# Kernel tuning notes

Measured on AMD Instinct MI355X. Metric: run time of the kernel, lower is better.

Reference implementation:

```python
import jax, jax.numpy as jnp
import numpy as np

N = 100000   # nodes
E = 1600000  # edges
D_IN = 4
D_H = 128
EPS = 1e-5

def setup_inputs() -> dict:
    key = jax.random.key(0)
    ks = jax.random.split(key, 4)
    x = jax.random.normal(ks[0], (N, D_IN), dtype=jnp.float32)
    edge_index = jax.random.randint(ks[1], (2, E), 0, N, dtype=jnp.int32)
    W0 = jax.random.normal(ks[2], (D_IN, D_H), dtype=jnp.float32) * 0.5
    b0 = jnp.zeros((D_H,), jnp.float32)
    W12 = jax.random.normal(ks[3], (2, D_H, D_H), dtype=jnp.float32) * (1.0 / np.sqrt(D_H))
    b12 = jnp.zeros((2, D_H), jnp.float32)
    gamma = jnp.ones((3, D_H), jnp.float32)   # GraphNorm weight
    beta = jnp.zeros((3, D_H), jnp.float32)   # GraphNorm bias
    alpha = jnp.ones((3, D_H), jnp.float32)   # GraphNorm mean_scale
    return dict(x=x, edge_index=edge_index, W0=W0, b0=b0, W12=W12, b12=b12,
                gamma=gamma, beta=beta, alpha=alpha)

def gcn_conv(x, src, dst, dinv, W, b):
    # PyG GCNConv: linear first, then D^-1/2 (A+I) D^-1/2 aggregation, bias after.
    h = x @ W                                  # [N, d_out]
    coef = dinv[src] * dinv[dst]               # [E]
    msg = h[src] * coef[:, None]               # [E, d_out] gather
    agg = jax.ops.segment_sum(msg, dst, num_segments=N)  # scatter-add
    agg = agg + h * (dinv * dinv)[:, None]     # self-loop contribution
    return agg + b

def graph_norm(x, g, be, a):
    # single-graph GraphNorm: gamma*(x - alpha*mu)/sqrt(E[(x-alpha*mu)^2]+eps)+beta
    mu = x.mean(axis=0)
    xc = x - a * mu
    var = (xc * xc).mean(axis=0)
    return g * xc * jax.lax.rsqrt(var + EPS) + be

def reference(x, edge_index, W0, b0, W12, b12, gamma, beta, alpha):
    src, dst = edge_index[0], edge_index[1]
    # degree with self loops (edge weight 1)
    deg = jax.ops.segment_sum(jnp.ones((E,), x.dtype), dst, num_segments=N) + 1.0
    dinv = jax.lax.rsqrt(deg)
    h = jax.nn.relu(graph_norm(gcn_conv(x, src, dst, dinv, W0, b0),
                               gamma[0], beta[0], alpha[0]))
    for i in range(2):  # fixed small layer loop
        h = jax.nn.relu(graph_norm(gcn_conv(h, src, dst, dinv, W12[i], b12[i]),
                                   gamma[i + 1], beta[i + 1], alpha[i + 1]))
    return h
```

## Files before the change

### kernel.cpp

```cpp
#include <hip/hip_runtime.h>


#define EPS_GN 1e-5f

typedef __attribute__((ext_vector_type(8))) short bf16x8;
typedef __attribute__((ext_vector_type(4))) float f32x4;

__device__ __forceinline__ float blo(unsigned u) { return __uint_as_float(u << 16); }
__device__ __forceinline__ float bhi(unsigned u) { return __uint_as_float(u & 0xffff0000u); }
__device__ __forceinline__ unsigned bf16rne(float f) {
  unsigned u = __float_as_uint(f);
  u += 0x7fff + ((u >> 16) & 1);
  return u >> 16;
}
__device__ __forceinline__ unsigned packbf(float x, float y) {
  return bf16rne(x) | (bf16rne(y) << 16);
}


__global__ __launch_bounds__(256) void k_count_p(const int* __restrict__ dst,
                                                 int* __restrict__ cnt, int E, int N) {
  int p = blockIdx.x & 7;
  int lo = (int)((long long)N * p >> 3), hi = (int)((long long)N * (p + 1) >> 3);
  int stride = (gridDim.x >> 3) * 256;
  for (int e = (blockIdx.x >> 3) * 256 + threadIdx.x; e < E; e += stride) {
    int d = dst[e];
    if (d >= lo && d < hi) atomicAdd(&cnt[d], 1);
  }
}

__global__ __launch_bounds__(256) void k_scan1(const int* __restrict__ cnt,
                                               int* __restrict__ rs,
                                               int* __restrict__ bsum, int N) {
  __shared__ int s[256];
  int t = threadIdx.x;
  int base = blockIdx.x * 1024 + t * 4;
  int c0 = (base + 0 < N) ? cnt[base + 0] : 0;
  int c1 = (base + 1 < N) ? cnt[base + 1] : 0;
  int c2 = (base + 2 < N) ? cnt[base + 2] : 0;
  int c3 = (base + 3 < N) ? cnt[base + 3] : 0;
  int tsum = c0 + c1 + c2 + c3;
  s[t] = tsum;
  __syncthreads();
  for (int off = 1; off < 256; off <<= 1) {
    int v = (t >= off) ? s[t - off] : 0;
    __syncthreads();
    s[t] += v;
    __syncthreads();
  }
  int excl = s[t] - tsum;
  if (t == 255) bsum[blockIdx.x] = s[255];
  int e0 = excl, e1 = e0 + c0, e2 = e1 + c1, e3 = e2 + c2;
  if (base + 0 < N) rs[base + 0] = e0;
  if (base + 1 < N) rs[base + 1] = e1;
  if (base + 2 < N) rs[base + 2] = e2;
  if (base + 3 < N) rs[base + 3] = e3;
}

__global__ __launch_bounds__(256) void k_scan2(const int* __restrict__ bsum,
                                               int* __restrict__ boff, int nblk) {
  __shared__ int s[256];
  int t = threadIdx.x;
  int v0 = (t < nblk) ? bsum[t] : 0;
  s[t] = v0;
  __syncthreads();
  for (int off = 1; off < 256; off <<= 1) {
    int v = (t >= off) ? s[t - off] : 0;
    __syncthreads();
    s[t] += v;
    __syncthreads();
  }
  if (t < nblk) boff[t] = s[t] - v0;
}

__global__ __launch_bounds__(256) void k_finalize(const int* __restrict__ cnt,
                                                  const int* __restrict__ boff,
                                                  int* __restrict__ rs,
                                                  int* __restrict__ cursor,
                                                  float* __restrict__ dinv,
                                                  unsigned* __restrict__ Hcb, int N, int E,
                                                  int ROWS) {
  int i = blockIdx.x * 256 + threadIdx.x;
  if (i == 0) rs[N] = E;
  if (i < 64) Hcb[((size_t)(i >> 3) * ROWS + N) * 8 + (i & 7)] = 0u;
  if (i < N) {
    int v = rs[i] + boff[i >> 10];
    rs[i] = v;
    cursor[i] = v;
    dinv[i] = rsqrtf((float)cnt[i] + 1.0f);
  }
}

__global__ __launch_bounds__(256) void k_fill_p(const int* __restrict__ src,
                                                const int* __restrict__ dst,
                                                int* __restrict__ cursor,
                                                int* __restrict__ csr, int E, int N) {
  int p = blockIdx.x & 7;
  int lo = (int)((long long)N * p >> 3), hi = (int)((long long)N * (p + 1) >> 3);
  int stride = (gridDim.x >> 3) * 256;
  for (int e = (blockIdx.x >> 3) * 256 + threadIdx.x; e < E; e += stride) {
    int d = dst[e];
    if (d >= lo && d < hi) {
      int pos = atomicAdd(&cursor[d], 1);
      csr[pos] = src[e];
    }
  }
}


__global__ __launch_bounds__(256) void k_wt(const float* __restrict__ W12,
                                            unsigned short* __restrict__ WbT) {
  int o = blockIdx.x * 256 + threadIdx.x;
  int layer = o >> 14, r = o & 16383;
  int n = r >> 7, k = r & 127;
  WbT[o] = (unsigned short)bf16rne(W12[layer * 16384 + k * 128 + n]);
}


__global__ __launch_bounds__(256) void k_gemm0(const float* __restrict__ X,
                                               const float* __restrict__ W,
                                               const float* __restrict__ dinv,
                                               unsigned* __restrict__ Hcb, int N, int ROWS) {
  __shared__ float Ws[4 * 128];
  int t = threadIdx.x;
  if (t < 128) {
    Ws[t] = W[t];
    Ws[128 + t] = W[128 + t];
    Ws[256 + t] = W[256 + t];
    Ws[384 + t] = W[384 + t];
  }
  __syncthreads();
  int r = t >> 6, l = t & 63;
  int row = blockIdx.x * 4 + r;
  if (row >= N) return;
  float4 xv = ((const float4*)X)[row];
  float di = dinv[row];
  int c0 = 2 * l, c1 = 2 * l + 1;
  float v0 = xv.x * Ws[c0] + xv.y * Ws[128 + c0] + xv.z * Ws[256 + c0] + xv.w * Ws[384 + c0];
  float v1 = xv.x * Ws[c1] + xv.y * Ws[128 + c1] + xv.z * Ws[256 + c1] + xv.w * Ws[384 + c1];
  Hcb[((size_t)(l >> 3) * ROWS + row) * 8 + (l & 7)] = packbf(di * v0, di * v1);
}

__global__ __launch_bounds__(256, 4) void k_gemm_mfma(const unsigned* __restrict__ AGGcb,
                                                      const unsigned short* __restrict__ WbT,
                                                      const float* __restrict__ stats,
                                                      const float* __restrict__ bias,
                                                      const float* __restrict__ gamma,
                                                      const float* __restrict__ beta,
                                                      const float* __restrict__ alpha,
                                                      const float* __restrict__ dinv,
                                                      unsigned* __restrict__ Hcb, int N,
                                                      int ROWS, float invN) {
  __shared__ float As[128], Bs[128];
  int t = threadIdx.x;
  if (t < 128) {
    float s1 = stats[t] * invN, s2 = stats[128 + t] * invN;
    float b = bias[t], a = alpha[t], g = gamma[t], be = beta[t];
    float mu = s1 + b;
    float E2 = s2 + 2.f * b * s1 + b * b;
    float var = E2 - (2.f * a - a * a) * mu * mu;
    float A = g * rsqrtf(var + EPS_GN);
    As[t] = A;
    Bs[t] = be - A * a * mu + A * b;
  }
  __syncthreads();
  int wv = t >> 6, l = t & 63;
  int r0 = blockIdx.x * 64 + wv * 16;
  if (r0 >= N) return;
  int m = l & 15, kb = l >> 4;

  f32x4 acc[8];
#pragma unroll
  for (int nt = 0; nt < 8; ++nt) acc[nt] = (f32x4){0.f, 0.f, 0.f, 0.f};

#pragma unroll
  for (int ks = 0; ks < 4; ++ks) {
    int k0 = ks * 32 + kb * 8;
    const uint4* pa = (const uint4*)(AGGcb + ((size_t)(2 * ks + (kb >> 1)) * ROWS + r0 + m) * 8 +
                                     (kb & 1) * 4);
    uint4 a_raw = pa[0];
    float4 A0 = *reinterpret_cast<const float4*>(&As[k0]);
    float4 A1 = *reinterpret_cast<const float4*>(&As[k0 + 4]);
    float4 B0 = *reinterpret_cast<const float4*>(&Bs[k0]);
    float4 B1 = *reinterpret_cast<const float4*>(&Bs[k0 + 4]);
    bf16x8 bf[8];
#pragma unroll
    for (int nt = 0; nt < 8; ++nt)
      bf[nt] = *reinterpret_cast<const bf16x8*>(WbT + (size_t)(nt * 16 + m) * 128 + k0);
    float xr[8] = {blo(a_raw.x), bhi(a_raw.x), blo(a_raw.y), bhi(a_raw.y),
                   blo(a_raw.z), bhi(a_raw.z), blo(a_raw.w), bhi(a_raw.w)};
    float Aa[8] = {A0.x, A0.y, A0.z, A0.w, A1.x, A1.y, A1.z, A1.w};
    float Bb[8] = {B0.x, B0.y, B0.z, B0.w, B1.x, B1.y, B1.z, B1.w};
    bf16x8 af;
#pragma unroll
    for (int j = 0; j < 8; ++j) {
      float v = fmaf(Aa[j], xr[j], Bb[j]);
      v = v > 0.f ? v : 0.f;
      af[j] = (short)bf16rne(v);
    }
#pragma unroll
    for (int nt = 0; nt < 8; ++nt)
      acc[nt] = __builtin_amdgcn_mfma_f32_16x16x32_bf16(af, bf[nt], acc[nt], 0, 0, 0);
  }

  float dn[4];
#pragma unroll
  for (int r = 0; r < 4; ++r) dn[r] = dinv[r0 + kb * 4 + r];
  bool even = (l & 1) == 0;
#pragma unroll
  for (int nt = 0; nt < 8; ++nt) {
#pragma unroll
    for (int r = 0; r < 4; ++r) {
      float v = acc[nt][r] * dn[r];
      float pv = __shfl_xor(v, 1);
      if (even) {
        unsigned word = packbf(v, pv);
        Hcb[((size_t)nt * ROWS + r0 + kb * 4 + r) * 8 + (m >> 1)] = word;
      }
    }
  }
}

__global__ __launch_bounds__(256) void k_gather_cb(const unsigned* __restrict__ Hcb,
                                                   const int* __restrict__ rs,
                                                   const int* __restrict__ csr,
                                                   const float* __restrict__ dinv,
                                                   unsigned* __restrict__ AGGcb,
                                                   float* __restrict__ stats, int N, int ROWS) {
  int t = threadIdx.x;
  int wave = t >> 6, lane = t & 63;
  int g = lane >> 4, e = (lane >> 1) & 7, h = lane & 1;
  int p = blockIdx.x & 7;
  const uint4* Hp4 = (const uint4*)(Hcb + (size_t)p * ROWS * 8);
  uint4* Ap4 = (uint4*)(AGGcb + (size_t)p * ROWS * 8);
  int q = blockIdx.x >> 3;
  int nstride = (gridDim.x >> 3) * 16;
  float s1acc[8], s2acc[8];
#pragma unroll
  for (int i = 0; i < 8; ++i) s1acc[i] = s2acc[i] = 0.f;

  for (int n0 = (q * 4 + wave) * 4; n0 < N; n0 += nstride) {
    int n = n0 + g;
    int j0 = rs[n], j1 = rs[n + 1];
    int len = j1 - j0;
    int nb = (len + 8) >> 3;
    int ml = nb;
    ml = max(ml, __shfl_xor(ml, 16));
    ml = max(ml, __shfl_xor(ml, 32));
    float acc[8];
#pragma unroll
    for (int i = 0; i < 8; ++i) acc[i] = 0.f;

    auto ld = [&](int b) -> uint4 {
      int j = b * 8 + e - 1;
      int jj = j0 + j;
      jj = min(jj, j1 - 1);
      jj = max(jj, j0);
      int c = csr[jj];
      int r = (j < 0) ? n : ((j < len) ? c : N);
      return Hp4[(size_t)r * 2 + h];
    };

    uint4 rA = ld(0);
    uint4 rB, rC, rD, rE;
    if (ml > 1) rB = ld(1);
    if (ml > 2) rC = ld(2);
    if (ml > 3) rD = ld(3);
    for (int b = 0; b < ml; ++b) {
      if (b + 4 < ml) rE = ld(b + 4);
      unsigned uu[4] = {rA.x, rA.y, rA.z, rA.w};
#pragma unroll
      for (int i = 0; i < 4; ++i) {
        acc[2 * i] += blo(uu[i]);
        acc[2 * i + 1] += bhi(uu[i]);
      }
      rA = rB;
      rB = rC;
      rC = rD;
      rD = rE;
    }
#pragma unroll
    for (int i = 0; i < 8; ++i) {
      acc[i] += __shfl_xor(acc[i], 2);
      acc[i] += __shfl_xor(acc[i], 4);
      acc[i] += __shfl_xor(acc[i], 8);
    }
    if (e == 0) {
      float dn = dinv[n];
      float v[8];
      uint4 wv;
      unsigned* wp = (unsigned*)&wv;
#pragma unroll
      for (int i = 0; i < 8; ++i) v[i] = acc[i] * dn;
#pragma unroll
      for (int i = 0; i < 4; ++i) wp[i] = packbf(v[2 * i], v[2 * i + 1]);
      Ap4[(size_t)n * 2 + h] = wv;
#pragma unroll
      for (int i = 0; i < 8; ++i) {
        s1acc[i] += v[i];
        s2acc[i] = fmaf(v[i], v[i], s2acc[i]);
      }
    }
  }
#pragma unroll
  for (int i = 0; i < 8; ++i) {
    s1acc[i] += __shfl_xor(s1acc[i], 16);
    s1acc[i] += __shfl_xor(s1acc[i], 32);
    s2acc[i] += __shfl_xor(s2acc[i], 16);
    s2acc[i] += __shfl_xor(s2acc[i], 32);
  }
  __shared__ float sh[4][32];
  if (lane < 2) {
#pragma unroll
    for (int i = 0; i < 8; ++i) {
      sh[wave][h * 8 + i] = s1acc[i];
      sh[wave][16 + h * 8 + i] = s2acc[i];
    }
  }
  __syncthreads();
  if (t < 32) {
    float v = sh[0][t] + sh[1][t] + sh[2][t] + sh[3][t];
    if (t < 16)
      atomicAdd(&stats[p * 16 + t], v);
    else
      atomicAdd(&stats[128 + p * 16 + (t - 16)], v);
  }
}

__global__ __launch_bounds__(256) void k_norm(const unsigned* __restrict__ AGGcb,
                                              const float* __restrict__ stats,
                                              const float* __restrict__ bias,
                                              const float* __restrict__ gamma,
                                              const float* __restrict__ beta,
                                              const float* __restrict__ alpha,
                                              float* __restrict__ OUT, int N, int ROWS,
                                              float invN) {
  int i = blockIdx.x * 256 + threadIdx.x;
  if (i >= N * 32) return;
  int row = i >> 5, c4 = i & 31;
  int blk = c4 >> 2, off = (2 * c4) & 7;
  uint2 u = *(const uint2*)(AGGcb + ((size_t)blk * ROWS + row) * 8 + off);
  float vv[4] = {blo(u.x), bhi(u.x), blo(u.y), bhi(u.y)};
  float ov[4];
#pragma unroll
  for (int j = 0; j < 4; ++j) {
    int c = c4 * 4 + j;
    float s1 = stats[c] * invN, s2 = stats[128 + c] * invN;
    float b = bias[c], a = alpha[c], g = gamma[c], be = beta[c];
    float mu = s1 + b;
    float E2 = s2 + 2.f * b * s1 + b * b;
    float var = E2 - (2.f * a - a * a) * mu * mu;
    float A = g * rsqrtf(var + EPS_GN);
    float B = be - A * a * mu + A * b;
    float o = fmaf(A, vv[j], B);
    ov[j] = o > 0.f ? o : 0.f;
  }
  ((float4*)OUT)[i] = make_float4(ov[0], ov[1], ov[2], ov[3]);
}


extern "C" void kernel_launch(void* const* d_in, const int* in_sizes, int n_in,
                              void* d_out, int out_size, void* d_ws, size_t ws_size,
                              hipStream_t stream) {
  const float* x = (const float*)d_in[0];
  const int* ei = (const int*)d_in[1];
  const float* W0 = (const float*)d_in[2];
  const float* b0 = (const float*)d_in[3];
  const float* W12 = (const float*)d_in[4];
  const float* b12 = (const float*)d_in[5];
  const float* gamma = (const float*)d_in[6];
  const float* beta = (const float*)d_in[7];
  const float* alpha = (const float*)d_in[8];
  float* out = (float*)d_out;

  int N = in_sizes[0] / 4;
  int E = in_sizes[1] / 2;
  int ROWS = N + 1;
  const int* srcArr = ei;
  const int* dstArr = ei + E;

  char* w = (char*)d_ws;
  auto alloc = [&](size_t bytes) {
    char* p = w;
    w += (bytes + 255) & ~(size_t)255;
    return p;
  };
  int* cnt = (int*)alloc((size_t)N * 4);
  float* stats = (float*)alloc(3 * 256 * 4);
  int* rs = (int*)alloc(((size_t)N + 1) * 4);
  int* cursor = (int*)alloc((size_t)N * 4);
  int* bsum = (int*)alloc(512);
  int* boff = (int*)alloc(512);
  unsigned short* WbT = (unsigned short*)alloc(2 * 16384 * 2);
  int* csr = (int*)alloc(((size_t)E + 8) * 4);
  float* dinv = (float*)alloc((size_t)N * 4);
  unsigned* Hcb = (unsigned*)alloc((size_t)ROWS * 64 * 4);
  unsigned* AGGcb = (unsigned*)alloc((size_t)ROWS * 64 * 4);

  size_t zlen = (size_t)((char*)stats - (char*)cnt) + 3 * 256 * 4;
  hipMemsetAsync(cnt, 0, zlen, stream);

  int nblk = (N + 1023) / 1024;
  k_wt<<<128, 256, 0, stream>>>(W12, WbT);
  k_count_p<<<2048, 256, 0, stream>>>(dstArr, cnt, E, N);
  k_scan1<<<nblk, 256, 0, stream>>>(cnt, rs, bsum, N);
  k_scan2<<<1, 256, 0, stream>>>(bsum, boff, nblk);
  k_finalize<<<(N + 255) / 256, 256, 0, stream>>>(cnt, boff, rs, cursor, dinv, Hcb, N, E, ROWS);
  k_fill_p<<<2048, 256, 0, stream>>>(srcArr, dstArr, cursor, csr, E, N);

  float invN = 1.0f / (float)N;
  int gGemm = (N + 63) / 64;

  k_gemm0<<<(N + 3) / 4, 256, 0, stream>>>(x, W0, dinv, Hcb, N, ROWS);
  k_gather_cb<<<2048, 256, 0, stream>>>(Hcb, rs, csr, dinv, AGGcb, stats, N, ROWS);
  k_gemm_mfma<<<gGemm, 256, 0, stream>>>(AGGcb, WbT, stats, b0, gamma, beta, alpha, dinv, Hcb, N,
                                         ROWS, invN);
  k_gather_cb<<<2048, 256, 0, stream>>>(Hcb, rs, csr, dinv, AGGcb, stats + 256, N, ROWS);
  k_gemm_mfma<<<gGemm, 256, 0, stream>>>(AGGcb, WbT + 16384, stats + 256, b12, gamma + 128,
                                         beta + 128, alpha + 128, dinv, Hcb, N, ROWS, invN);
  k_gather_cb<<<2048, 256, 0, stream>>>(Hcb, rs, csr, dinv, AGGcb, stats + 512, N, ROWS);
  k_norm<<<(N * 32 + 255) / 256, 256, 0, stream>>>(AGGcb, stats + 512, b12 + 128, gamma + 256,
                                                   beta + 256, alpha + 256, out, N, ROWS, invN);
}
```

Before: 720.1 us.

## Pad CSR rows to multiples of eight with self-loop and sentinel entries

```diff
diff --git a/kernel.cpp b/kernel.cpp
--- a/kernel.cpp
+++ b/kernel.cpp
@@ -35,10 +35,10 @@
   __shared__ int s[256];
   int t = threadIdx.x;
   int base = blockIdx.x * 1024 + t * 4;
-  int c0 = (base + 0 < N) ? cnt[base + 0] : 0;
-  int c1 = (base + 1 < N) ? cnt[base + 1] : 0;
-  int c2 = (base + 2 < N) ? cnt[base + 2] : 0;
-  int c3 = (base + 3 < N) ? cnt[base + 3] : 0;
+  int c0 = (base + 0 < N) ? ((cnt[base + 0] + 8) & ~7) : 0;
+  int c1 = (base + 1 < N) ? ((cnt[base + 1] + 8) & ~7) : 0;
+  int c2 = (base + 2 < N) ? ((cnt[base + 2] + 8) & ~7) : 0;
+  int c3 = (base + 3 < N) ? ((cnt[base + 3] + 8) & ~7) : 0;
   int tsum = c0 + c1 + c2 + c3;
   s[t] = tsum;
   __syncthreads();
@@ -78,23 +78,37 @@
                                                   int* __restrict__ rs,
                                                   int* __restrict__ cursor,
                                                   float* __restrict__ dinv,
-                                                  unsigned* __restrict__ Hcb, int N, int E,
+                                                  unsigned* __restrict__ Hcb,
+                                                  int* __restrict__ csrp, int N, int E,
                                                   int ROWS) {
+  __shared__ int sTail;
   int i = blockIdx.x * 256 + threadIdx.x;
-  if (i == 0) rs[N] = E;
   if (i < 64) Hcb[((size_t)(i >> 3) * ROWS + N) * 8 + (i & 7)] = 0u;
   if (i < N) {
     int v = rs[i] + boff[i >> 10];
+    int c = cnt[i];
+    int pc = (c + 8) & ~7;
     rs[i] = v;
-    cursor[i] = v;
-    dinv[i] = rsqrtf((float)cnt[i] + 1.0f);
+    cursor[i] = v + 1;
+    dinv[i] = rsqrtf((float)c + 1.0f);
+    csrp[v] = i;
+    for (int k = v + 1 + c; k < v + pc; ++k) csrp[k] = N;
+    if (i == N - 1) {
+      rs[N] = v + pc;
+      sTail = v + pc;
+    }
+  }
+  __syncthreads();
+  if (blockIdx.x == gridDim.x - 1) {
+    int base = sTail;
+    for (int k = threadIdx.x; k < 1024; k += 256) csrp[base + k] = N;
   }
 }
 
 __global__ __launch_bounds__(256) void k_fill_p(const int* __restrict__ src,
                                                 const int* __restrict__ dst,
                                                 int* __restrict__ cursor,
-                                                int* __restrict__ csr, int E, int N) {
+                                                int* __restrict__ csrp, int E, int N) {
   int p = blockIdx.x & 7;
   int lo = (int)((long long)N * p >> 3), hi = (int)((long long)N * (p + 1) >> 3);
   int stride = (gridDim.x >> 3) * 256;
@@ -102,7 +116,7 @@
     int d = dst[e];
     if (d >= lo && d < hi) {
       int pos = atomicAdd(&cursor[d], 1);
-      csr[pos] = src[e];
+      csrp[pos] = src[e];
     }
   }
 }
@@ -222,8 +236,8 @@
 }
 
 __global__ __launch_bounds__(256) void k_gather_cb(const unsigned* __restrict__ Hcb,
-                                                   const int* __restrict__ rs,
-                                                   const int* __restrict__ csr,
+                                                   const int* __restrict__ rsp,
+                                                   const int* __restrict__ csrp,
                                                    const float* __restrict__ dinv,
                                                    unsigned* __restrict__ AGGcb,
                                                    float* __restrict__ stats, int N, int ROWS) {
@@ -241,9 +255,8 @@
 
   for (int n0 = (q * 4 + wave) * 4; n0 < N; n0 += nstride) {
     int n = n0 + g;
-    int j0 = rs[n], j1 = rs[n + 1];
-    int len = j1 - j0;
-    int nb = (len + 8) >> 3;
+    int j0 = rsp[n], j1 = rsp[n + 1];
+    int nb = (j1 - j0) >> 3;
     int ml = nb;
     ml = max(ml, __shfl_xor(ml, 16));
     ml = max(ml, __shfl_xor(ml, 32));
@@ -251,33 +264,39 @@
 #pragma unroll
     for (int i = 0; i < 8; ++i) acc[i] = 0.f;
 
-    auto ld = [&](int b) -> uint4 {
-      int j = b * 8 + e - 1;
-      int jj = j0 + j;
-      jj = min(jj, j1 - 1);
-      jj = max(jj, j0);
-      int c = csr[jj];
-      int r = (j < 0) ? n : ((j < len) ? c : N);
-      return Hp4[(size_t)r * 2 + h];
+    const int* cp = csrp + j0 + e;
+    auto hload = [&](int c, int b) -> uint4 {
+      int ce = (b < nb) ? c : N;
+      return Hp4[(size_t)ce * 2 + h];
     };
-
-    uint4 rA = ld(0);
-    uint4 rB, rC, rD, rE;
-    if (ml > 1) rB = ld(1);
-    if (ml > 2) rC = ld(2);
-    if (ml > 3) rD = ld(3);
-    for (int b = 0; b < ml; ++b) {
-      if (b + 4 < ml) rE = ld(b + 4);
-      unsigned uu[4] = {rA.x, rA.y, rA.z, rA.w};
-#pragma unroll
-      for (int i = 0; i < 4; ++i) {
-        acc[2 * i] += blo(uu[i]);
-        acc[2 * i + 1] += bhi(uu[i]);
+    int c0 = cp[0], c1 = cp[8];
+    uint4 hA = hload(c0, 0);
+    uint4 hB = hload(c1, 1);
+    int c2 = cp[16], c3 = cp[24];
+    const int* cpp = cp + 32;
+
+    for (int b = 0; b < ml; b += 2) {
+      {
+        unsigned uu[4] = {hA.x, hA.y, hA.z, hA.w};
+#pragma unroll
+        for (int i = 0; i < 4; ++i) {
+          acc[2 * i] += blo(uu[i]);
+          acc[2 * i + 1] += bhi(uu[i]);
+        }
       }
-      rA = rB;
-      rB = rC;
-      rC = rD;
-      rD = rE;
+      hA = hload(c2, b + 2);
+      c2 = cpp[0];
+      if (b + 1 < ml) {
+        unsigned uu[4] = {hB.x, hB.y, hB.z, hB.w};
+#pragma unroll
+        for (int i = 0; i < 4; ++i) {
+          acc[2 * i] += blo(uu[i]);
+          acc[2 * i + 1] += bhi(uu[i]);
+        }
+        hB = hload(c3, b + 3);
+        c3 = cpp[8];
+      }
+      cpp += 16;
     }
 #pragma unroll
     for (int i = 0; i < 8; ++i) {
@@ -392,7 +411,7 @@
   int* bsum = (int*)alloc(512);
   int* boff = (int*)alloc(512);
   unsigned short* WbT = (unsigned short*)alloc(2 * 16384 * 2);
-  int* csr = (int*)alloc(((size_t)E + 8) * 4);
+  int* csrp = (int*)alloc(((size_t)E + 8 * (size_t)N + 2048) * 4);
   float* dinv = (float*)alloc((size_t)N * 4);
   unsigned* Hcb = (unsigned*)alloc((size_t)ROWS * 64 * 4);
   unsigned* AGGcb = (unsigned*)alloc((size_t)ROWS * 64 * 4);
@@ -405,20 +424,21 @@
   k_count_p<<<2048, 256, 0, stream>>>(dstArr, cnt, E, N);
   k_scan1<<<nblk, 256, 0, stream>>>(cnt, rs, bsum, N);
   k_scan2<<<1, 256, 0, stream>>>(bsum, boff, nblk);
-  k_finalize<<<(N + 255) / 256, 256, 0, stream>>>(cnt, boff, rs, cursor, dinv, Hcb, N, E, ROWS);
-  k_fill_p<<<2048, 256, 0, stream>>>(srcArr, dstArr, cursor, csr, E, N);
+  k_finalize<<<(N + 255) / 256, 256, 0, stream>>>(cnt, boff, rs, cursor, dinv, Hcb, csrp, N, E,
+                                                  ROWS);
+  k_fill_p<<<2048, 256, 0, stream>>>(srcArr, dstArr, cursor, csrp, E, N);
 
   float invN = 1.0f / (float)N;
   int gGemm = (N + 63) / 64;
 
   k_gemm0<<<(N + 3) / 4, 256, 0, stream>>>(x, W0, dinv, Hcb, N, ROWS);
-  k_gather_cb<<<2048, 256, 0, stream>>>(Hcb, rs, csr, dinv, AGGcb, stats, N, ROWS);
+  k_gather_cb<<<2048, 256, 0, stream>>>(Hcb, rs, csrp, dinv, AGGcb, stats, N, ROWS);
   k_gemm_mfma<<<gGemm, 256, 0, stream>>>(AGGcb, WbT, stats, b0, gamma, beta, alpha, dinv, Hcb, N,
                                          ROWS, invN);
-  k_gather_cb<<<2048, 256, 0, stream>>>(Hcb, rs, csr, dinv, AGGcb, stats + 256, N, ROWS);
+  k_gather_cb<<<2048, 256, 0, stream>>>(Hcb, rs, csrp, dinv, AGGcb, stats + 256, N, ROWS);
   k_gemm_mfma<<<gGemm, 256, 0, stream>>>(AGGcb, WbT + 16384, stats + 256, b12, gamma + 128,
                                          beta + 128, alpha + 128, dinv, Hcb, N, ROWS, invN);
-  k_gather_cb<<<2048, 256, 0, stream>>>(Hcb, rs, csr, dinv, AGGcb, stats + 512, N, ROWS);
+  k_gather_cb<<<2048, 256, 0, stream>>>(Hcb, rs, csrp, dinv, AGGcb, stats + 512, N, ROWS);
   k_norm<<<(N * 32 + 255) / 256, 256, 0, stream>>>(AGGcb, stats + 512, b12 + 128, gamma + 256,
                                                    beta + 256, alpha + 256, out, N, ROWS, invN);
 }
```

After: 696.8 us. 1.03x faster.
